# Performance work log

Measured on AMD Instinct MI355X. Metric: run time of the kernel, lower is better.

Reference implementation:

```python
import jax, jax.numpy as jnp
import numpy as np

N_QUBITS = 12
N_LAYERS = 4
BATCH = 4096
OUT_DIM = 12


def _ry(theta):
    theta = jnp.asarray(theta, jnp.float32)
    c, s = jnp.cos(theta / 2), jnp.sin(theta / 2)
    U = jnp.stack([jnp.stack([c, -s], -1), jnp.stack([s, c], -1)], -2)
    return U.astype(jnp.complex64)


def _rx(theta):
    theta = jnp.asarray(theta, jnp.float32)
    c = jnp.cos(theta / 2).astype(jnp.complex64)
    s = (-1j) * jnp.sin(theta / 2).astype(jnp.complex64)
    return jnp.stack([jnp.stack([c, s], -1), jnp.stack([s, c], -1)], -2)


def _rz(theta):
    theta = jnp.asarray(theta, jnp.float32)
    e = jnp.exp((-0.5j) * theta.astype(jnp.complex64))
    z = jnp.zeros_like(e)
    return jnp.stack([jnp.stack([e, z], -1), jnp.stack([z, jnp.conj(e)], -1)], -2)


def _apply_1q(psi, U, w):
    # psi: (B,) + (2,)*n; U: (2,2) shared gate or (B,2,2) per-sample gate
    psi = jnp.moveaxis(psi, w + 1, 1)
    if U.ndim == 2:
        psi = jnp.einsum('ij,bj...->bi...', U, psi)
    else:
        psi = jnp.einsum('bij,bj...->bi...', U, psi)
    return jnp.moveaxis(psi, 1, w + 1)


def _cnot(psi, c, t):
    # flip target axis where control bit == 1
    psi = jnp.moveaxis(psi, (c + 1, t + 1), (1, 2))
    psi = psi.at[:, 1].set(psi[:, 1, ::-1])
    return jnp.moveaxis(psi, (1, 2), (c + 1, t + 1))


def _pauli_z_signs(n):
    idx = np.arange(2 ** n)
    bits = (idx[None, :] >> (n - 1 - np.arange(n))[:, None]) & 1  # wire 0 = MSB
    return jnp.asarray(1.0 - 2.0 * bits, jnp.float32)  # (n, 2^n)


def _quantum_forward(x, quantum_weights):
    b, n = x.shape[0], N_QUBITS
    # tf.nn.l2_normalize(sample, axis=0) per sample
    xn = x * jax.lax.rsqrt(jnp.maximum(jnp.sum(x * x, axis=1, keepdims=True), 1e-12))
    # angle encoding: pi * x / (max|x| + 1e-8)
    angles = jnp.pi * xn / (jnp.max(jnp.abs(xn), axis=1, keepdims=True) + 1e-8)
    psi = jnp.zeros((b, 2 ** n), jnp.complex64).at[:, 0].set(1.0)
    psi = psi.reshape((b,) + (2,) * n)
    # data encoding: RY(angles[i]) on wire i (per-sample batched gates)
    for i in range(n):
        psi = _apply_1q(psi, _ry(angles[:, i]), i)
    # variational layers: RX/RY/RZ per qubit, then CNOT ring
    for layer in range(N_LAYERS):
        base = layer * 3 * n
        for i in range(n):
            p = base + 3 * i
            psi = _apply_1q(psi, _rx(quantum_weights[p]), i)
            psi = _apply_1q(psi, _ry(quantum_weights[p + 1]), i)
            psi = _apply_1q(psi, _rz(quantum_weights[p + 2]), i)
        for i in range(n):
            psi = _cnot(psi, i, (i + 1) % n)
    psi = psi.reshape(b, -1)
    probs = jnp.real(psi) ** 2 + jnp.imag(psi) ** 2  # (B, 2^n)
    return probs @ _pauli_z_signs(n).T  # (B, n): <Z_i> per qubit


def setup_inputs() -> dict:
    key = jax.random.key(0)
    k1, k2, k3 = jax.random.split(key, 3)
    n_params = 3 * N_QUBITS * N_LAYERS
    return {
        'x': jax.random.normal(k1, (BATCH, N_QUBITS), jnp.float32),
        'quantum_weights': jax.random.uniform(k2, (n_params,), jnp.float32, -0.05, 0.05),
        'dense_w': jax.random.normal(k3, (N_QUBITS, OUT_DIM), jnp.float32) / np.sqrt(N_QUBITS),
        'dense_b': jnp.zeros((OUT_DIM,), jnp.float32),
    }


def reference(x, quantum_weights, dense_w, dense_b):
    q = _quantum_forward(x, quantum_weights)
    return jnp.tanh(q @ dense_w + dense_b)
```

## Files before the change

### kernel.cpp

```cpp
#include <hip/hip_runtime.h>
#include <math.h>

#define NQ   12
#define NL   4
#define QBLK 512
#define SOFF(i) (8192 + (i) * 8192)

typedef float v4f  __attribute__((ext_vector_type(4)));
typedef __fp16 v8h __attribute__((ext_vector_type(8)));
typedef unsigned v4u __attribute__((ext_vector_type(4)));

__device__ __forceinline__ constexpr int sigma_inv_c(int i) {
    int j = i;
    for (int c = 0; c < NQ; ++c) {
        int t = (c + 1) % NQ;
        int cb = (j >> (NQ - 1 - c)) & 1;
        j ^= cb << (NQ - 1 - t);
    }
    return j;
}

__device__ __forceinline__ constexpr int lswz(int l) {
    return l ^ (((l >> 3) ^ (l >> 7)) & 7);
}

__device__ __forceinline__ unsigned pk2(float a, float b) {
    return __builtin_bit_cast(unsigned, __builtin_amdgcn_cvt_pkrtz(a, b));
}

__device__ __forceinline__ int fslot(int k, int n) {
    return ((k >> 3) * 16 + n) * 8 + (k & 7);
}

__device__ __forceinline__ v8h derive_b2(v8h b) {
    v4u w = __builtin_bit_cast(v4u, b);
    v4u r;
    #pragma unroll
    for (int i = 0; i < 4; ++i) {
        const unsigned rot = (w[i] >> 16) | (w[i] << 16);
        r[i] = rot ^ 0x8000u;
    }
    return __builtin_bit_cast(v8h, r);
}

#define READ_FRAGS(AF, SRC)                                                 \
    _Pragma("unroll")                                                       \
    for (int j = 0; j < 2; ++j)                                             \
        AF[j] = __builtin_bit_cast(v8h, *(const uint4*)&sh[(SRC) +          \
                    lswz((((wv) << 6) | ((2 * qh + j) << 4) | nn) * 4 + g) * 8]);

#define BLOAD(MAT)                                                          \
    const v8h b1 = *(const v8h*)&sh[(MAT) * 512 + lane * 8];                \
    const v8h b2 = derive_b2(b1);

#define BLOAD2(MATB, MATC)                                                  \
    const v8h b1 = *(const v8h*)&sh[(MATB) * 512 + lane * 8];               \
    const v8h b2 = derive_b2(b1);                                           \
    const v8h c1 = *(const v8h*)&sh[(MATC) * 512 + lane * 8];               \
    const v8h c2 = derive_b2(c1);

#define MFMA_ONE(AF)                                                        \
    _Pragma("unroll")                                                       \
    for (int j = 0; j < 2; ++j) {                                           \
        d1[j] = __builtin_amdgcn_mfma_f32_16x16x32_f16(AF[j], b1, zf, 0, 0, 0); \
        d2[j] = __builtin_amdgcn_mfma_f32_16x16x32_f16(AF[j], b2, zf, 0, 0, 0); \
    }

#define PACK_AF(AF)                                                         \
    _Pragma("unroll")                                                       \
    for (int j = 0; j < 2; ++j) {                                           \
        v4u t;                                                              \
        _Pragma("unroll")                                                   \
        for (int rg = 0; rg < 4; ++rg) t[rg] = pk2(d1[j][rg], d2[j][rg]);   \
        AF[j] = __builtin_bit_cast(v8h, t);                                 \
    }

#define MFMA_CC(AF)                                                         \
    _Pragma("unroll")                                                       \
    for (int j = 0; j < 2; ++j) {                                           \
        d1[j] = __builtin_amdgcn_mfma_f32_16x16x32_f16(AF[j], c1, zf, 0, 0, 0); \
        d2[j] = __builtin_amdgcn_mfma_f32_16x16x32_f16(AF[j], c2, zf, 0, 0, 0); \
    }

#define SCHB __builtin_amdgcn_sched_barrier(0);

#define COLS_ONE(AF, D1x, D2x, DST)                                         \
    _Pragma("unroll")                                                       \
    for (int j = 0; j < 2; ++j) {                                           \
        D1x[j] = __builtin_amdgcn_mfma_f32_16x16x32_f16(AF[j], b1, zf, 0, 0, 0); \
        D2x[j] = __builtin_amdgcn_mfma_f32_16x16x32_f16(AF[j], b2, zf, 0, 0, 0); \
    }                                                                       \
    _Pragma("unroll")                                                       \
    for (int j = 0; j < 2; ++j) {                                           \
        const int CCn = (nn << 4) | (wv << 2) | (2 * qh + j);               \
        *(uint4*)&sh[(DST) + lswz(CCn * 4 + g) * 8] =                       \
            make_uint4(pk2(D1x[j].x, D2x[j].x), pk2(D1x[j].y, D2x[j].y),    \
                       pk2(D1x[j].z, D2x[j].z), pk2(D1x[j].w, D2x[j].w));   \
    }

#define CHAIN_ONE(AF, D1x, D2x, DST)                                        \
    _Pragma("unroll")                                                       \
    for (int j = 0; j < 2; ++j) {                                           \
        D1x[j] = __builtin_amdgcn_mfma_f32_16x16x32_f16(AF[j], b1, zf, 0, 0, 0); \
        D2x[j] = __builtin_amdgcn_mfma_f32_16x16x32_f16(AF[j], b2, zf, 0, 0, 0); \
    }                                                                       \
    _Pragma("unroll")                                                       \
    for (int j = 0; j < 2; ++j) {                                           \
        v4u t;                                                              \
        _Pragma("unroll")                                                   \
        for (int rg = 0; rg < 4; ++rg) t[rg] = pk2(D1x[j][rg], D2x[j][rg]); \
        AF[j] = __builtin_bit_cast(v8h, t);                                 \
    }                                                                       \
    _Pragma("unroll")                                                       \
    for (int j = 0; j < 2; ++j) {                                           \
        D1x[j] = __builtin_amdgcn_mfma_f32_16x16x32_f16(AF[j], c1, zf, 0, 0, 0); \
        D2x[j] = __builtin_amdgcn_mfma_f32_16x16x32_f16(AF[j], c2, zf, 0, 0, 0); \
    }                                                                       \
    _Pragma("unroll")                                                       \
    for (int j = 0; j < 2; ++j) {                                           \
        const int ij = ifix2 ^ (j ? sigma_inv_c(1) : 0);                    \
        _Pragma("unroll")                                                   \
        for (int rg = 0; rg < 4; ++rg) {                                    \
            const int ii = ij ^ sigma_inv_c(rg << 4);                       \
            *(unsigned*)&sh[(DST) + lswz(ii >> 2) * 8 + (ii & 3) * 2] =     \
                pk2(D1x[j][rg], D2x[j][rg]);                                \
        }                                                                   \
    }

#define WHT_EPI2(OFF)                                                       \
    { float p8[8];                                                          \
      _Pragma("unroll")                                                     \
      for (int j = 0; j < 2; ++j)                                           \
          _Pragma("unroll")                                                 \
          for (int rg = 0; rg < 4; ++rg)                                    \
              p8[j * 4 + rg] = d1[j][rg] * d1[j][rg] + d2[j][rg] * d2[j][rg]; \
      _Pragma("unroll")                                                     \
      for (int st = 1; st < 8; st <<= 1) {                                  \
          _Pragma("unroll")                                                 \
          for (int i = 0; i < 8; ++i) {                                     \
              if (!(i & st)) {                                              \
                  const float a = p8[i], b = p8[i ^ st];                    \
                  p8[i] = a + b; p8[i ^ st] = a - b;                        \
              }                                                             \
          }                                                                 \
      }                                                                     \
      float vals[NQ];                                                       \
      _Pragma("unroll")                                                     \
      for (int w = 0; w < NQ; ++w) {                                        \
          const int sb = 11 - w;                                            \
          const int fj  = (sigma_inv_c(0x001) >> sb) & 1;                   \
          const int frh = (sigma_inv_c(0x020) >> sb) & 1;                   \
          const int frl = (sigma_inv_c(0x010) >> sb) & 1;                   \
          const float v = p8[fj * 4 + frh * 2 + frl];                       \
          vals[w] = ((ifix2 >> sb) & 1) ? -v : v;                           \
      }                                                                     \
      _Pragma("unroll")                                                     \
      for (int m = 1; m <= 8; m <<= 1) {                                    \
          _Pragma("unroll")                                                 \
          for (int w = 0; w < NQ; ++w) vals[w] += __shfl_xor(vals[w], m);   \
      }                                                                     \
      if ((lane & 15) == 0) {                                               \
          _Pragma("unroll")                                                 \
          for (int w = 0; w < NQ; ++w)                                      \
              red[(OFF) + W * 48 + (lane >> 4) * 12 + w] = vals[w];         \
      } }

__global__ __launch_bounds__(QBLK) void qsim_kernel(
    const float* __restrict__ x,
    const float* __restrict__ qw,
    const float* __restrict__ dw,
    const float* __restrict__ db,
    float* __restrict__ out,
    int batch)
{
    __shared__ __align__(16) __fp16 sh[40960];
    float* fb    = (float*)(sh + 6144);
    float* xv    = fb;
    float* enc_c = fb + 64;
    float* enc_s = fb + 128;
    float* Gt    = fb + 192;
    float* red   = (float*)(sh + SOFF(0));

    const int tid  = threadIdx.x;
    const int lane = tid & 63;
    const int W    = tid >> 6;
    const int wv   = W & 3;
    const int qh   = W >> 2;
    const int base = 4 * blockIdx.x;
    int ss[4];
    #pragma unroll
    for (int i = 0; i < 4; ++i) {
        int s = base + i;
        ss[i] = (s < batch) ? s : batch - 1;
    }
    const int nn = lane & 15, g = lane >> 4;
    const v4f zf = {0.f, 0.f, 0.f, 0.f};

    if (tid < 4 * NQ) {
        const int smp = tid / NQ, j = tid - smp * NQ;
        xv[tid] = x[ss[smp] * NQ + j];
    }
    __syncthreads();
    if (tid < 4 * NQ) {
        const int b0 = (tid / NQ) * NQ;
        float sum = 0.f;
        #pragma unroll
        for (int j = 0; j < NQ; ++j) sum += xv[b0 + j] * xv[b0 + j];
        float inv = rsqrtf(fmaxf(sum, 1e-12f));
        float mx = 0.f;
        #pragma unroll
        for (int j = 0; j < NQ; ++j) mx = fmaxf(mx, fabsf(xv[b0 + j] * inv));
        float ang = 3.14159265358979323846f * (xv[tid] * inv) / (mx + 1e-8f);
        float cc, sn;
        sincosf(0.5f * ang, &sn, &cc);
        enc_c[tid] = cc; enc_s[tid] = sn;
    } else if (tid >= 64 && tid < 64 + NL * NQ) {
        const int t = tid - 64;
        const int p = (t / NQ) * 3 * NQ + 3 * (t % NQ);
        float t1 = qw[p], t2 = qw[p + 1], t3 = qw[p + 2];
        float a, b, c, d, gr, h;
        sincosf(0.5f * t1, &b, &a);
        sincosf(0.5f * t2, &d, &c);
        sincosf(0.5f * t3, &h, &gr);
        float m00r =  c * a, m00i =  d * b;
        float m01r = -d * a, m01i = -c * b;
        float m10r =  d * a, m10i = -c * b;
        float m11r =  c * a, m11i = -d * b;
        float* gg = Gt + t * 8;
        gg[0] = gr * m00r + h * m00i;  gg[1] = gr * m00i - h * m00r;
        gg[2] = gr * m01r + h * m01i;  gg[3] = gr * m01i - h * m01r;
        gg[4] = gr * m10r - h * m10i;  gg[5] = gr * m10i + h * m10r;
        gg[6] = gr * m11r - h * m11i;  gg[7] = gr * m11i + h * m11r;
    }
    __syncthreads();

    #pragma unroll
    for (int e = 0; e < 6; ++e) {
        const int idx = tid * 6 + e;
        const int mat = idx >> 8, rn = idx & 255;
        const int r = rn >> 4, n = rn & 15;
        const int layer = mat / 3, ph = mat - 3 * layer;
        const int wbase = (ph == 0) ? 8 : (ph == 1) ? 4 : 0;
        float cr = 1.f, ci = 0.f;
        #pragma unroll
        for (int b = 0; b < 4; ++b) {
            const float* gg = Gt + (layer * NQ + wbase + b) * 8;
            const int rb = (r >> (3 - b)) & 1, nb = (n >> (3 - b)) & 1;
            const float er = gg[(nb * 2 + rb) * 2], ei = gg[(nb * 2 + rb) * 2 + 1];
            const float xr = cr * er - ci * ei, xi = cr * ei + ci * er;
            cr = xr; ci = xi;
        }
        sh[mat * 512 + fslot(2 * r, n)]     = (__fp16)cr;
        sh[mat * 512 + fslot(2 * r + 1, n)] = (__fp16)(-ci);
    }

    v8h af0[2], af1[2], af2[2], af3[2];
    #define PICK(SMP, WW, B) ((B) ? enc_s[(SMP) * NQ + (WW)] : enc_c[(SMP) * NQ + (WW)])
    #define INIT_AF(AF, SMP)                                                \
    {   float R4[4];                                                        \
        _Pragma("unroll")                                                   \
        for (int t = 0; t < 4; ++t) {                                       \
            const int r = 4 * g + t;                                        \
            R4[t] = PICK(SMP, 8, (r >> 3) & 1) * PICK(SMP, 9, (r >> 2) & 1) \
                  * PICK(SMP, 10, (r >> 1) & 1) * PICK(SMP, 11, r & 1);     \
        }                                                                   \
        const float Pfix = PICK(SMP, 0, (wv >> 1) & 1) * PICK(SMP, 1, wv & 1) \
                         * PICK(SMP, 4, (nn >> 3) & 1) * PICK(SMP, 5, (nn >> 2) & 1) \
                         * PICK(SMP, 6, (nn >> 1) & 1) * PICK(SMP, 7, nn & 1); \
        _Pragma("unroll")                                                   \
        for (int j = 0; j < 2; ++j) {                                       \
            const float Pq = Pfix * PICK(SMP, 2, qh) * PICK(SMP, 3, j);     \
            _Pragma("unroll")                                               \
            for (int t = 0; t < 4; ++t) {                                   \
                AF[j][2 * t]     = (__fp16)(Pq * R4[t]);                    \
                AF[j][2 * t + 1] = (__fp16)0.f;                             \
            }                                                               \
        }                                                                   \
    }
    INIT_AF(af0, 0)
    INIT_AF(af1, 1)
    INIT_AF(af2, 2)
    INIT_AF(af3, 3)
    #undef PICK
    __syncthreads();

    const int ifix2 = sigma_inv_c((nn << 8) | (g << 6) | (wv << 2) | (qh << 1));

    v4f d1[2], d2[2], e1[2], e2[2], f1[2], f2[2], h1[2], h2[2];
    #define READ4                                                           \
        READ_FRAGS(af0, SOFF(0)) READ_FRAGS(af1, SOFF(1))                   \
        READ_FRAGS(af2, SOFF(2)) READ_FRAGS(af3, SOFF(3))
    #define COLS4(MAT)                                                      \
        { BLOAD(MAT)                                                        \
          COLS_ONE(af0, d1, d2, SOFF(0))                                    \
          COLS_ONE(af1, e1, e2, SOFF(1))                                    \
          COLS_ONE(af2, f1, f2, SOFF(2))                                    \
          COLS_ONE(af3, h1, h2, SOFF(3)) }
    #define CHAIN4(MATB, MATC)                                              \
        { BLOAD2(MATB, MATC)                                                \
          CHAIN_ONE(af0, d1, d2, SOFF(0))                                   \
          CHAIN_ONE(af1, e1, e2, SOFF(1))                                   \
          CHAIN_ONE(af2, f1, f2, SOFF(2))                                   \
          CHAIN_ONE(af3, h1, h2, SOFF(3)) }
    #define CHAIN_E(AF)                                                     \
        MFMA_ONE(AF)                                                        \
        _Pragma("unroll")                                                   \
        for (int j = 0; j < 2; ++j) {                                       \
            v4u t;                                                          \
            _Pragma("unroll")                                               \
            for (int rg = 0; rg < 4; ++rg) t[rg] = pk2(d1[j][rg], d2[j][rg]); \
            AF[j] = __builtin_bit_cast(v8h, t);                             \
        }                                                                   \
        _Pragma("unroll")                                                   \
        for (int j = 0; j < 2; ++j) {                                       \
            d1[j] = __builtin_amdgcn_mfma_f32_16x16x32_f16(AF[j], c1, zf, 0, 0, 0); \
            d2[j] = __builtin_amdgcn_mfma_f32_16x16x32_f16(AF[j], c2, zf, 0, 0, 0); \
        }

    #pragma unroll 1
    for (int l = 0; l < NL; ++l) {
        if (l > 0) {
            READ4
            __syncthreads();
        }
        COLS4(l * 3 + 0)
        __syncthreads();

        READ4
        __syncthreads();
        if (l < NL - 1) {
            CHAIN4(l * 3 + 1, l * 3 + 2)
            __syncthreads();
        } else {
            { BLOAD2(l * 3 + 1, l * 3 + 2)
              CHAIN_E(af0) WHT_EPI2(0)    SCHB
              CHAIN_E(af1) WHT_EPI2(384)  SCHB
              CHAIN_E(af2) WHT_EPI2(768)  SCHB
              CHAIN_E(af3) WHT_EPI2(1152) }
        }
    }

    __syncthreads();
    if (tid < 4 * NQ) {
        const int smp = tid / NQ, w = tid - smp * NQ;
        float acc = 0.f;
        #pragma unroll
        for (int k = 0; k < 32; ++k) acc += red[smp * 384 + k * 12 + w];
        red[1536 + tid] = acc;
    }
    __syncthreads();
    if (tid < 4 * NQ) {
        const int smp = tid / NQ, o = tid - smp * NQ;
        const float* rv = red + 1536 + smp * NQ;
        float v = db[o];
        #pragma unroll
        for (int w = 0; w < NQ; ++w) v += rv[w] * dw[w * NQ + o];
        out[ss[smp] * NQ + o] = tanhf(v);
    }
}

extern "C" void kernel_launch(void* const* d_in, const int* in_sizes, int n_in,
                              void* d_out, int out_size, void* d_ws, size_t ws_size,
                              hipStream_t stream) {
    const float* x  = (const float*)d_in[0];
    const float* qw = (const float*)d_in[1];
    const float* dw = (const float*)d_in[2];
    const float* db = (const float*)d_in[3];
    float* out = (float*)d_out;
    int batch = in_sizes[0] / NQ;
    int nblk = (batch + 3) / 4;
    qsim_kernel<<<nblk, QBLK, 0, stream>>>(x, qw, dw, db, out, batch);
}
```

Measured before the change: 107.7 us.

## Halve samples per block and double-buffer state to drop barriers

Each block now simulates 2 samples instead of 4, launching twice as many blocks. Shared memory is split into two ping-pong buffers per sample (SB0/SB1), so fragment reads and writes go to different buffers and two __syncthreads per layer can be removed. This targets barrier stalls and the per-block register footprint, which should raise occupancy. The cost is more blocks with repeated setup work (gate matrix construction, encoding) per sample.

```diff
diff --git a/kernel.cpp b/kernel.cpp
--- a/kernel.cpp
+++ b/kernel.cpp
@@ -4,7 +4,8 @@
 #define NQ   12
 #define NL   4
 #define QBLK 512
-#define SOFF(i) (8192 + (i) * 8192)
+#define SB0(s) (8192 + (s) * 16384)
+#define SB1(s) (16384 + (s) * 16384)
 
 typedef float v4f  __attribute__((ext_vector_type(4)));
 typedef __fp16 v8h __attribute__((ext_vector_type(8)));
@@ -66,22 +67,6 @@
         d2[j] = __builtin_amdgcn_mfma_f32_16x16x32_f16(AF[j], b2, zf, 0, 0, 0); \
     }
 
-#define PACK_AF(AF)                                                         \
-    _Pragma("unroll")                                                       \
-    for (int j = 0; j < 2; ++j) {                                           \
-        v4u t;                                                              \
-        _Pragma("unroll")                                                   \
-        for (int rg = 0; rg < 4; ++rg) t[rg] = pk2(d1[j][rg], d2[j][rg]);   \
-        AF[j] = __builtin_bit_cast(v8h, t);                                 \
-    }
-
-#define MFMA_CC(AF)                                                         \
-    _Pragma("unroll")                                                       \
-    for (int j = 0; j < 2; ++j) {                                           \
-        d1[j] = __builtin_amdgcn_mfma_f32_16x16x32_f16(AF[j], c1, zf, 0, 0, 0); \
-        d2[j] = __builtin_amdgcn_mfma_f32_16x16x32_f16(AF[j], c2, zf, 0, 0, 0); \
-    }
-
 #define SCHB __builtin_amdgcn_sched_barrier(0);
 
 #define COLS_ONE(AF, D1x, D2x, DST)                                         \
@@ -125,6 +110,21 @@
             *(unsigned*)&sh[(DST) + lswz(ii >> 2) * 8 + (ii & 3) * 2] =     \
                 pk2(D1x[j][rg], D2x[j][rg]);                                \
         }                                                                   \
+    }
+
+#define CHAIN_E(AF)                                                         \
+    MFMA_ONE(AF)                                                            \
+    _Pragma("unroll")                                                       \
+    for (int j = 0; j < 2; ++j) {                                           \
+        v4u t;                                                              \
+        _Pragma("unroll")                                                   \
+        for (int rg = 0; rg < 4; ++rg) t[rg] = pk2(d1[j][rg], d2[j][rg]);   \
+        AF[j] = __builtin_bit_cast(v8h, t);                                 \
+    }                                                                       \
+    _Pragma("unroll")                                                       \
+    for (int j = 0; j < 2; ++j) {                                           \
+        d1[j] = __builtin_amdgcn_mfma_f32_16x16x32_f16(AF[j], c1, zf, 0, 0, 0); \
+        d2[j] = __builtin_amdgcn_mfma_f32_16x16x32_f16(AF[j], c2, zf, 0, 0, 0); \
     }
 
 #define WHT_EPI2(OFF)                                                       \
@@ -179,29 +179,29 @@
     float* enc_c = fb + 64;
     float* enc_s = fb + 128;
     float* Gt    = fb + 192;
-    float* red   = (float*)(sh + SOFF(0));
+    float* red   = (float*)(sh + SB0(0));
 
     const int tid  = threadIdx.x;
     const int lane = tid & 63;
     const int W    = tid >> 6;
     const int wv   = W & 3;
     const int qh   = W >> 2;
-    const int base = 4 * blockIdx.x;
-    int ss[4];
+    const int base = 2 * blockIdx.x;
+    int ss[2];
     #pragma unroll
-    for (int i = 0; i < 4; ++i) {
+    for (int i = 0; i < 2; ++i) {
         int s = base + i;
         ss[i] = (s < batch) ? s : batch - 1;
     }
     const int nn = lane & 15, g = lane >> 4;
     const v4f zf = {0.f, 0.f, 0.f, 0.f};
 
-    if (tid < 4 * NQ) {
+    if (tid < 2 * NQ) {
         const int smp = tid / NQ, j = tid - smp * NQ;
         xv[tid] = x[ss[smp] * NQ + j];
     }
     __syncthreads();
-    if (tid < 4 * NQ) {
+    if (tid < 2 * NQ) {
         const int b0 = (tid / NQ) * NQ;
         float sum = 0.f;
         #pragma unroll
@@ -254,7 +254,7 @@
         sh[mat * 512 + fslot(2 * r + 1, n)] = (__fp16)(-ci);
     }
 
-    v8h af0[2], af1[2], af2[2], af3[2];
+    v8h af0[2], af1[2];
     #define PICK(SMP, WW, B) ((B) ? enc_s[(SMP) * NQ + (WW)] : enc_c[(SMP) * NQ + (WW)])
     #define INIT_AF(AF, SMP)                                                \
     {   float R4[4];                                                        \
@@ -279,79 +279,49 @@
     }
     INIT_AF(af0, 0)
     INIT_AF(af1, 1)
-    INIT_AF(af2, 2)
-    INIT_AF(af3, 3)
     #undef PICK
     __syncthreads();
 
     const int ifix2 = sigma_inv_c((nn << 8) | (g << 6) | (wv << 2) | (qh << 1));
 
-    v4f d1[2], d2[2], e1[2], e2[2], f1[2], f2[2], h1[2], h2[2];
-    #define READ4                                                           \
-        READ_FRAGS(af0, SOFF(0)) READ_FRAGS(af1, SOFF(1))                   \
-        READ_FRAGS(af2, SOFF(2)) READ_FRAGS(af3, SOFF(3))
-    #define COLS4(MAT)                                                      \
-        { BLOAD(MAT)                                                        \
-          COLS_ONE(af0, d1, d2, SOFF(0))                                    \
-          COLS_ONE(af1, e1, e2, SOFF(1))                                    \
-          COLS_ONE(af2, f1, f2, SOFF(2))                                    \
-          COLS_ONE(af3, h1, h2, SOFF(3)) }
-    #define CHAIN4(MATB, MATC)                                              \
-        { BLOAD2(MATB, MATC)                                                \
-          CHAIN_ONE(af0, d1, d2, SOFF(0))                                   \
-          CHAIN_ONE(af1, e1, e2, SOFF(1))                                   \
-          CHAIN_ONE(af2, f1, f2, SOFF(2))                                   \
-          CHAIN_ONE(af3, h1, h2, SOFF(3)) }
-    #define CHAIN_E(AF)                                                     \
-        MFMA_ONE(AF)                                                        \
-        _Pragma("unroll")                                                   \
-        for (int j = 0; j < 2; ++j) {                                       \
-            v4u t;                                                          \
-            _Pragma("unroll")                                               \
-            for (int rg = 0; rg < 4; ++rg) t[rg] = pk2(d1[j][rg], d2[j][rg]); \
-            AF[j] = __builtin_bit_cast(v8h, t);                             \
-        }                                                                   \
-        _Pragma("unroll")                                                   \
-        for (int j = 0; j < 2; ++j) {                                       \
-            d1[j] = __builtin_amdgcn_mfma_f32_16x16x32_f16(AF[j], c1, zf, 0, 0, 0); \
-            d2[j] = __builtin_amdgcn_mfma_f32_16x16x32_f16(AF[j], c2, zf, 0, 0, 0); \
-        }
-
+    v4f d1[2], d2[2], e1[2], e2[2];
     #pragma unroll 1
     for (int l = 0; l < NL; ++l) {
         if (l > 0) {
-            READ4
-            __syncthreads();
+            READ_FRAGS(af0, SB0(0))
+            READ_FRAGS(af1, SB0(1))
         }
-        COLS4(l * 3 + 0)
+        { BLOAD(l * 3 + 0)
+          COLS_ONE(af0, d1, d2, SB1(0))
+          COLS_ONE(af1, e1, e2, SB1(1)) }
         __syncthreads();
 
-        READ4
-        __syncthreads();
+        READ_FRAGS(af0, SB1(0))
+        READ_FRAGS(af1, SB1(1))
         if (l < NL - 1) {
-            CHAIN4(l * 3 + 1, l * 3 + 2)
+            { BLOAD2(l * 3 + 1, l * 3 + 2)
+              CHAIN_ONE(af0, d1, d2, SB0(0))
+              CHAIN_ONE(af1, e1, e2, SB0(1)) }
             __syncthreads();
         } else {
             { BLOAD2(l * 3 + 1, l * 3 + 2)
-              CHAIN_E(af0) WHT_EPI2(0)    SCHB
-              CHAIN_E(af1) WHT_EPI2(384)  SCHB
-              CHAIN_E(af2) WHT_EPI2(768)  SCHB
-              CHAIN_E(af3) WHT_EPI2(1152) }
+              CHAIN_E(af0) WHT_EPI2(0)   SCHB
+              CHAIN_E(af1) WHT_EPI2(384) }
         }
     }
 
     __syncthreads();
-    if (tid < 4 * NQ) {
+    if (tid < 2 * NQ) {
         const int smp = tid / NQ, w = tid - smp * NQ;
         float acc = 0.f;
         #pragma unroll
         for (int k = 0; k < 32; ++k) acc += red[smp * 384 + k * 12 + w];
-        red[1536 + tid] = acc;
-    }
-    __syncthreads();
-    if (tid < 4 * NQ) {
+        red[768 + tid] = acc;
+    }
+    __syncthreads();
+    if (tid < 2 * NQ) {
         const int smp = tid / NQ, o = tid - smp * NQ;
-        const float* rv = red + 1536 + smp * NQ;
+        const float* rv = red + 768 + smp * NQ;
         float v = db[o];
         #pragma unroll
         for (int w = 0; w < NQ; ++w) v += rv[w] * dw[w * NQ + o];
@@ -368,6 +338,6 @@
     const float* db = (const float*)d_in[3];
     float* out = (float*)d_out;
     int batch = in_sizes[0] / NQ;
-    int nblk = (batch + 3) / 4;
+    int nblk = (batch + 1) / 2;
     qsim_kernel<<<nblk, QBLK, 0, stream>>>(x, qw, dw, db, out, batch);
 }
```

Result: slower. 115.2 us (+7.0%).
